# Kernel tuning notes

Measured on AMD Instinct MI355X. Metric: run time of the kernel, lower is better.

## Reference

```python
import jax, jax.numpy as jnp
import numpy as np

N_HEADS = 16

def setup_inputs() -> dict:
    key = jax.random.key(0)
    k1, k2, k3 = jax.random.split(key, 3)
    B, L, D = 2, 2048, 1024
    x = jax.random.normal(k1, (B, L, D), dtype=jnp.float32)
    w_qkv = jax.random.normal(k2, (D, 3 * D), dtype=jnp.float32) * (1.0 / np.sqrt(D))
    w_out = jax.random.normal(k3, (D, D), dtype=jnp.float32) * (1.0 / np.sqrt(D))
    return {"x": x, "w_qkv": w_qkv, "w_out": w_out}

def reference(x, w_qkv, w_out):
    B, L, D = x.shape
    H = N_HEADS
    dh = D // H
    qkv = x @ w_qkv                      # (B, L, 3D)
    q, k, v = jnp.split(qkv, 3, axis=-1)
    # (B, H, L, dh)
    q = q.reshape(B, L, H, dh).transpose(0, 2, 1, 3)
    k = k.reshape(B, L, H, dh).transpose(0, 2, 1, 3)
    v = v.reshape(B, L, H, dh).transpose(0, 2, 1, 3)
    scale = 1.0 / jnp.sqrt(jnp.asarray(dh, x.dtype))
    attn = jnp.einsum('bhqd,bhkd->bhqk', q, k) * scale   # (B, H, L, L)
    causal = jnp.tril(jnp.ones((L, L), dtype=bool))
    attn = jnp.where(causal[None, None], attn, -jnp.inf)
    attn = jax.nn.softmax(attn, axis=-1)
    out = jnp.einsum('bhqk,bhkd->bhqd', attn, v)         # (B, H, L, dh)
    out = out.transpose(0, 2, 1, 3).reshape(B, L, D)
    return out @ w_out
```

## Files before the change

### kernel.cpp

```cpp
#include <hip/hip_runtime.h>

typedef __attribute__((ext_vector_type(4))) float f32x4;
typedef __attribute__((ext_vector_type(16))) float f32x16;
typedef __attribute__((ext_vector_type(8))) __bf16 bf16x8;
typedef __attribute__((ext_vector_type(4))) __bf16 bf16x4;
typedef __attribute__((ext_vector_type(4))) unsigned u32x4;
typedef __attribute__((ext_vector_type(2))) unsigned u32x2;

static __device__ __forceinline__ f32x4 mfma16(bf16x8 a, bf16x8 b, f32x4 c) {
    return __builtin_amdgcn_mfma_f32_16x16x32_bf16(a, b, c, 0, 0, 0);
}
static __device__ __forceinline__ f32x16 mfma32(bf16x8 a, bf16x8 b, f32x16 c) {
    return __builtin_amdgcn_mfma_f32_32x32x16_bf16(a, b, c, 0, 0, 0);
}
static __device__ __forceinline__ unsigned pk_bf16(float a, float b) {
    unsigned lo = __builtin_bit_cast(unsigned short, (__bf16)a);
    unsigned hh = __builtin_bit_cast(unsigned short, (__bf16)b);
    return lo | (hh << 16);
}

#define QSCALE 0.18033688f
#define FENCE() asm volatile("" ::: "memory")
#define SYNCB()                          \
    do {                                 \
        FENCE();                         \
        __builtin_amdgcn_s_barrier();    \
        FENCE();                         \
    } while (0)

__global__ __launch_bounds__(256) void prep_all(const float* __restrict__ x,
                                                __bf16* __restrict__ xb,
                                                const float* __restrict__ wq,
                                                __bf16* __restrict__ wqT,
                                                const float* __restrict__ wo,
                                                __bf16* __restrict__ woT) {
    __shared__ float t[32][33];
    int bid = blockIdx.x, tid = threadIdx.x;
    if (bid < 4096) {
        int i = bid * 256 + tid;
        f32x4 v = ((const f32x4*)x)[i];
        bf16x4 o;
#pragma unroll
        for (int j = 0; j < 4; j++) o[j] = (__bf16)v[j];
        ((bf16x4*)xb)[i] = o;
        return;
    }
    const float* in;
    __bf16* out;
    int R, C, bx, by;
    if (bid < 4096 + 3072) {
        int b2 = bid - 4096;
        in = wq; out = wqT; R = 1024; C = 3072;
        bx = (b2 % 96) * 32; by = (b2 / 96) * 32;
    } else {
        int b2 = bid - 7168;
        in = wo; out = woT; R = 1024; C = 1024;
        bx = (b2 % 32) * 32; by = (b2 / 32) * 32;
    }
    int tx = tid & 31, ty = tid >> 5;
#pragma unroll
    for (int k = 0; k < 32; k += 8)
        t[ty + k][tx] = in[(size_t)(by + ty + k) * C + bx + tx];
    __syncthreads();
#pragma unroll
    for (int k = 0; k < 32; k += 8)
        out[(size_t)(bx + ty + k) * R + by + tx] = (__bf16)t[tx][ty + k];
}

__global__ __launch_bounds__(512, 2) void qkv_gemm8(const __bf16* __restrict__ A,
                                                    const __bf16* __restrict__ Bt,
                                                    __bf16* __restrict__ Qf,
                                                    __bf16* __restrict__ Kf,
                                                    __bf16* __restrict__ Vf) {
    const int K = 1024, NT = 16, MT = 12;
    __shared__ __attribute__((aligned(16))) __bf16 smem[65536];
    int tid = threadIdx.x;
    int w = tid >> 6, lane = tid & 63;
    int lrow = lane & 15, lgrp = lane >> 4;
    int wm = w >> 2, wn = w & 3;
    int bid = blockIdx.x;
    int swz = (bid & 7) * 24 + (bid >> 3);
    int m0 = (swz % MT) * 256, n0 = (swz / MT) * 256;

    int schunk = ((lane & 3) ^ ((lane >> 3) & 3)) * 8;
    const __bf16* aS[2];
    const __bf16* bS[2];
    int dstRow[2];
#pragma unroll
    for (int l = 0; l < 2; l++) {
        int r = w * 32 + l * 16 + (lane >> 2);
        aS[l] = A + (size_t)(m0 + r) * K + schunk;
        bS[l] = Bt + (size_t)(n0 + r) * K + schunk;
        dstRow[l] = (w * 32 + l * 16) * 64;
    }

    auto STAGE = [&](int h, int tt) {
        int tc = tt < NT ? tt : NT - 1;
        int op = h & 1, kh = h >> 1;
        int base = ((tt & 1) << 16) + (kh << 15) + (op << 14);
#pragma unroll
        for (int l = 0; l < 2; l++) {
            const __bf16* src = (op ? bS[l] : aS[l]) + tc * 64 + kh * 32;
            __builtin_amdgcn_global_load_lds(
                (const __attribute__((address_space(1))) void*)src,
                (__attribute__((address_space(3))) void*)(smem +
                                                          ((base + dstRow[l]) >> 1)),
                16, 0, 0);
        }
    };

    int swzsel = (lgrp ^ ((lrow >> 1) & 3)) << 4;
    auto RDA = [&](int buf, int kk, int row) {
        int off = (buf << 16) + (kk << 15) + row * 64 + swzsel;
        return *(const bf16x8*)(smem + (off >> 1));
    };
    auto RDB = [&](int buf, int kk, int row) {
        int off = (buf << 16) + (kk << 15) + 16384 + row * 64 + swzsel;
        return *(const bf16x8*)(smem + (off >> 1));
    };

    f32x4 acc[8][4];
#pragma unroll
    for (int i = 0; i < 8; i++)
#pragma unroll
        for (int j = 0; j < 4; j++) acc[i][j] = (f32x4){0.f, 0.f, 0.f, 0.f};
    bf16x8 bfr[4];

    STAGE(0, 0); STAGE(1, 0); STAGE(2, 0); STAGE(3, 0);
    STAGE(0, 1); STAGE(1, 1);
    asm volatile("s_waitcnt vmcnt(8)" ::: "memory");
    SYNCB();

#define PH(T, KKv, MHv, SH, ST, DOVM)                                          \
    {                                                                          \
        bf16x8 af[4];                                                          \
        if (MHv == 0) {                                                        \
            _Pragma("unroll") for (int nt = 0; nt < 4; nt++) bfr[nt] =         \
                RDB((T) & 1, KKv, wn * 64 + nt * 16 + lrow);                   \
        }                                                                      \
        _Pragma("unroll") for (int i = 0; i < 4; i++) af[i] =                  \
            RDA((T) & 1, KKv, wm * 128 + (MHv * 4 + i) * 16 + lrow);           \
        STAGE(SH, ST);                                                         \
        if (DOVM) asm volatile("s_waitcnt vmcnt(8)" ::: "memory");             \
        SYNCB();                                                               \
        asm volatile("s_waitcnt lgkmcnt(0)" ::: "memory");                     \
        __builtin_amdgcn_sched_barrier(0);                                     \
        __builtin_amdgcn_s_setprio(1);                                         \
        _Pragma("unroll") for (int i = 0; i < 4; i++)                          \
            _Pragma("unroll") for (int nt = 0; nt < 4; nt++)                   \
                acc[MHv * 4 + i][nt] =                                         \
                    mfma16(af[i], bfr[nt], acc[MHv * 4 + i][nt]);              \
        __builtin_amdgcn_s_setprio(0);                                         \
        SYNCB();                                                               \
    }

#pragma unroll 2
    for (int t = 0; t < NT; ++t) {
        PH(t, 0, 0, 2, t + 1, 0);
        PH(t, 0, 1, 3, t + 1, 1);
        PH(t, 1, 0, 0, t + 2, 0);
        PH(t, 1, 1, 1, t + 2, 1);
    }
#undef PH

    asm volatile("s_waitcnt vmcnt(0)" ::: "memory");
    SYNCB();

#pragma unroll
    for (int mt = 0; mt < 8; mt++) {
#pragma unroll
        for (int nt = 0; nt < 4; nt++) {
            int f0 = m0 + wm * 128 + mt * 16 + lgrp * 4;
            int t = n0 + wn * 64 + nt * 16 + lrow;
            int which = f0 >> 10, hn = f0 & 1023;
            int h = hn >> 6, d0 = hn & 63;
            int b = t >> 11, li = t & 2047;
            int bh = b * 16 + h, c = li >> 5, tl = li & 31;
            size_t bhbase = (size_t)bh * 131072;
            if (which == 2) {
                int ks = tl >> 4, hv = (tl >> 3) & 1, jv = tl & 7;
                size_t base =
                    bhbase + ((size_t)(c * 4 + ks * 2 + hv) * 64 + d0) * 8 + jv;
#pragma unroll
                for (int r = 0; r < 4; r++)
                    Vf[base + (size_t)r * 8] = (__bf16)acc[mt][nt][r];
            } else {
                int st = d0 >> 4, hv = (d0 >> 3) & 1, j0 = d0 & 7;
                size_t idx =
                    bhbase + ((size_t)(c * 8 + st * 2 + hv) * 32 + tl) * 8 + j0;
                bf16x4 pv;
                if (which == 0) {
#pragma unroll
                    for (int r = 0; r < 4; r++)
                        pv[r] = (__bf16)(acc[mt][nt][r] * QSCALE);
                    *(bf16x4*)(Qf + idx) = pv;
                } else {
#pragma unroll
                    for (int r = 0; r < 4; r++) pv[r] = (__bf16)acc[mt][nt][r];
                    *(bf16x4*)(Kf + idx) = pv;
                }
            }
        }
    }
}

#define BN 128
#define BKG 64

template <int MODE, int BMv>
__global__ __launch_bounds__(256) void gemm_bt(const __bf16* __restrict__ A,
                                               const __bf16* __restrict__ Bt,
                                               int M, int N, int K,
                                               float* __restrict__ Cout) {
    constexpr int nMt = BMv / 32;
    __shared__ __attribute__((aligned(16))) __bf16 As[BMv * BKG];
    __shared__ __attribute__((aligned(16))) __bf16 Bs[BN * BKG];
    int tid = threadIdx.x;
    int wave = tid >> 6, lane = tid & 63;
    int lrow = lane & 15, lgrp = lane >> 4;
    int bid = blockIdx.x;
    int chunk = gridDim.x >> 3;
    int swz = (bid & 7) * chunk + (bid >> 3);
    int nbx = N >> 7;
    int m0 = (swz / nbx) * BMv;
    int n0 = (swz % nbx) * BN;
    int wm = (wave >> 1) * (BMv / 2);
    int wn = (wave & 1) * 64;

    f32x4 acc[nMt][4];
#pragma unroll
    for (int i = 0; i < nMt; i++)
#pragma unroll
        for (int j = 0; j < 4; j++) acc[i][j] = (f32x4){0.f, 0.f, 0.f, 0.f};

    int srow = tid >> 3;
    int gch = (tid & 7) ^ (srow & 7);
    const __bf16* aSrc = A + (size_t)(m0 + srow) * K + gch * 8;
    const __bf16* bSrc = Bt + (size_t)(n0 + srow) * K + gch * 8;

    for (int k0 = 0; k0 < K; k0 += BKG) {
#pragma unroll
        for (int c = 0; c < BMv / 32; c++) {
            __builtin_amdgcn_global_load_lds(
                (const __attribute__((address_space(1))) void*)(aSrc + k0 + (size_t)c * 32 * K),
                (__attribute__((address_space(3))) void*)(As + (c * 256 + wave * 64) * 8),
                16, 0, 0);
        }
#pragma unroll
        for (int c = 0; c < 4; c++) {
            __builtin_amdgcn_global_load_lds(
                (const __attribute__((address_space(1))) void*)(bSrc + k0 + (size_t)c * 32 * K),
                (__attribute__((address_space(3))) void*)(Bs + (c * 256 + wave * 64) * 8),
                16, 0, 0);
        }
        __syncthreads();
#pragma unroll
        for (int kk = 0; kk < 2; kk++) {
            bf16x8 af[nMt], bfr[4];
#pragma unroll
            for (int mt = 0; mt < nMt; mt++) {
                int row = wm + mt * 16 + lrow;
                int slot = row * 8 + ((4 * kk + lgrp) ^ (row & 7));
                af[mt] = *(const bf16x8*)(As + slot * 8);
            }
#pragma unroll
            for (int nt = 0; nt < 4; nt++) {
                int row = wn + nt * 16 + lrow;
                int slot = row * 8 + ((4 * kk + lgrp) ^ (row & 7));
                bfr[nt] = *(const bf16x8*)(Bs + slot * 8);
            }
#pragma unroll
            for (int mt = 0; mt < nMt; mt++)
#pragma unroll
                for (int nt = 0; nt < 4; nt++)
                    acc[mt][nt] = mfma16(af[mt], bfr[nt], acc[mt][nt]);
        }
        __syncthreads();
    }

#pragma unroll
    for (int mt = 0; mt < nMt; mt++) {
#pragma unroll
        for (int nt = 0; nt < 4; nt++) {
            int f0 = m0 + wm + mt * 16 + lgrp * 4;
            int t = n0 + wn + nt * 16 + lrow;
            *(f32x4*)(Cout + (size_t)t * M + f0) = acc[mt][nt];
        }
    }
}

template <bool MASKED>
static __device__ __forceinline__ void attn_chunk(
    int c, int ql, int hi, const __bf16* __restrict__ Kp,
    const __bf16* __restrict__ Vp, const bf16x8 (&qf)[4], bf16x8 ones,
    f32x16& o0, f32x16& o1, f32x16& lsa) {
    const __bf16* kb = Kp + ((size_t)c * 8 + hi) * 256 + ql * 8;
    bf16x8 kf[4];
#pragma unroll
    for (int st = 0; st < 4; st++) kf[st] = *(const bf16x8*)(kb + st * 512);
    const __bf16* vb = Vp + ((size_t)c * 4 + hi) * 512 + ql * 8;
    bf16x8 v00 = *(const bf16x8*)(vb);
    bf16x8 v01 = *(const bf16x8*)(vb + 256);
    bf16x8 v10 = *(const bf16x8*)(vb + 1024);
    bf16x8 v11 = *(const bf16x8*)(vb + 1280);

    f32x16 sa;
#pragma unroll
    for (int r = 0; r < 16; r++) sa[r] = 0.f;
#pragma unroll
    for (int st = 0; st < 4; st++) sa = mfma32(kf[st], qf[st], sa);

    unsigned w[8];
#pragma unroll
    for (int i = 0; i < 8; i++) {
        float a = sa[2 * i], b = sa[2 * i + 1];
        if (MASKED) {
            int ra = 2 * i, rb = 2 * i + 1;
            if (((ra & 3) + 8 * (ra >> 2) + 4 * hi) > ql) a = -1e30f;
            if (((rb & 3) + 8 * (rb >> 2) + 4 * hi) > ql) b = -1e30f;
        }
        w[i] = pk_bf16(__builtin_amdgcn_exp2f(a), __builtin_amdgcn_exp2f(b));
    }
    u32x2 r02 = __builtin_amdgcn_permlane32_swap(w[0], w[2], false, false);
    u32x2 r13 = __builtin_amdgcn_permlane32_swap(w[1], w[3], false, false);
    u32x2 r46 = __builtin_amdgcn_permlane32_swap(w[4], w[6], false, false);
    u32x2 r57 = __builtin_amdgcn_permlane32_swap(w[5], w[7], false, false);
    bf16x8 pa0 = __builtin_bit_cast(bf16x8, (u32x4){r02[0], r13[0], r02[1], r13[1]});
    bf16x8 pa1 = __builtin_bit_cast(bf16x8, (u32x4){r46[0], r57[0], r46[1], r57[1]});

    o0 = mfma32(pa0, v00, o0);
    o1 = mfma32(pa0, v01, o1);
    lsa = mfma32(pa0, ones, lsa);
    o0 = mfma32(pa1, v10, o0);
    o1 = mfma32(pa1, v11, o1);
    lsa = mfma32(pa1, ones, lsa);
}

__global__ __launch_bounds__(256, 4) void attn_fwd15(const __bf16* __restrict__ Qf,
                                                     const __bf16* __restrict__ Kf,
                                                     const __bf16* __restrict__ Vf,
                                                     __bf16* __restrict__ Ob) {
    __shared__ float comb[2][64][49];
    int tid = threadIdx.x;
    int wave = tid >> 6, lane = tid & 63;
    int ql = lane & 31, hi = lane >> 5;
    int bid = blockIdx.x;
    int xcd = bid & 7, idx = bid >> 3;
    int bh = xcd * 4 + (idx >> 6);
    int strip = 63 - (idx & 63);
    int q0 = strip * 32;

    const __bf16* Qp = Qf + (size_t)bh * 131072;
    const __bf16* Kp = Kf + (size_t)bh * 131072;
    const __bf16* Vp = Vf + (size_t)bh * 131072;

    const __bf16* qb = Qp + ((size_t)strip * 8 + hi) * 256 + ql * 8;
    bf16x8 qf[4];
#pragma unroll
    for (int st = 0; st < 4; st++) qf[st] = *(const bf16x8*)(qb + st * 512);

    bf16x8 ones;
#pragma unroll
    for (int j = 0; j < 8; j++) ones[j] = (__bf16)1.0f;

    f32x16 o0, o1, lsa;
#pragma unroll
    for (int r = 0; r < 16; r++) { o0[r] = 0.f; o1[r] = 0.f; lsa[r] = 0.f; }

    for (int c = wave; c < strip; c += 4)
        attn_chunk<false>(c, ql, hi, Kp, Vp, qf, ones, o0, o1, lsa);
    if ((strip & 3) == wave)
        attn_chunk<true>(strip, ql, hi, Kp, Vp, qf, ones, o0, o1, lsa);

    if (wave >= 2) {
        float* sl = &comb[wave - 2][lane][0];
#pragma unroll
        for (int r = 0; r < 16; r++) {
            sl[r] = o0[r]; sl[16 + r] = o1[r]; sl[32 + r] = lsa[r];
        }
    }
    __syncthreads();
    if (wave < 2) {
        const float* sl = &comb[wave][lane][0];
#pragma unroll
        for (int r = 0; r < 16; r++) {
            o0[r] += sl[r]; o1[r] += sl[16 + r]; lsa[r] += sl[32 + r];
        }
    }
    __syncthreads();
    if (wave == 1) {
        float* sl = &comb[0][lane][0];
#pragma unroll
        for (int r = 0; r < 16; r++) {
            sl[r] = o0[r]; sl[16 + r] = o1[r]; sl[32 + r] = lsa[r];
        }
    }
    __syncthreads();
    if (wave == 0) {
        const float* sl = &comb[0][lane][0];
#pragma unroll
        for (int r = 0; r < 16; r++) {
            o0[r] += sl[r]; o1[r] += sl[16 + r]; lsa[r] += sl[32 + r];
        }
        int b = bh >> 4, h = bh & 15;
#pragma unroll
        for (int r = 0; r < 16; r++) {
            int crow = (r & 3) + 8 * (r >> 2) + 4 * hi;
            float inv;
            asm("v_rcp_f32 %0, %1" : "=v"(inv) : "v"(lsa[r]));
            size_t base = ((size_t)(b * 2048 + q0 + crow)) * 1024 + h * 64;
            Ob[base + ql] = (__bf16)(o0[r] * inv);
            Ob[base + 32 + ql] = (__bf16)(o1[r] * inv);
        }
    }
}

extern "C" void kernel_launch(void* const* d_in, const int* in_sizes, int n_in,
                              void* d_out, int out_size, void* d_ws, size_t ws_size,
                              hipStream_t stream) {
    const float* x = (const float*)d_in[0];
    const float* w_qkv = (const float*)d_in[1];
    const float* w_out = (const float*)d_in[2];
    float* out = (float*)d_out;

    char* ws = (char*)d_ws;
    __bf16* xb    = (__bf16*)(ws);
    __bf16* wqkvT = (__bf16*)(ws + (size_t)(8  << 20));
    __bf16* woutT = (__bf16*)(ws + (size_t)(14 << 20));
    __bf16* Qf    = (__bf16*)(ws + (size_t)(16 << 20));
    __bf16* Kf    = (__bf16*)(ws + (size_t)(24 << 20));
    __bf16* Vf    = (__bf16*)(ws + (size_t)(32 << 20));
    __bf16* Ob    = (__bf16*)(ws + (size_t)(40 << 20));

    prep_all<<<8192, 256, 0, stream>>>(x, xb, w_qkv, wqkvT, w_out, woutT);
    qkv_gemm8<<<192, 512, 0, stream>>>(wqkvT, xb, Qf, Kf, Vf);
    attn_fwd15<<<2048, 256, 0, stream>>>(Qf, Kf, Vf, Ob);
    gemm_bt<0, 64><<<512, 256, 0, stream>>>(
        woutT, Ob, 1024, 4096, 1024, out);
}
```

Baseline: 94.79 us.

## Process two query strips per attention block to reuse K/V fragments

Each attention block now handles two adjacent 32-row query strips, so every K/V chunk loaded from global memory feeds both strips' QK and PV matrix multiplies. The grid is halved, launch bounds drop to 2 blocks per CU, and the shared-memory reduction buffer doubles to combine both strips' accumulators. This targets K/V load traffic and per-block overhead, in exchange for higher register pressure, lower occupancy and coarser load balancing across the causal triangle.

```diff
diff --git a/kernel.cpp b/kernel.cpp
--- a/kernel.cpp
+++ b/kernel.cpp
@@ -290,20 +290,10 @@
 }
 
 template <bool MASKED>
-static __device__ __forceinline__ void attn_chunk(
-    int c, int ql, int hi, const __bf16* __restrict__ Kp,
-    const __bf16* __restrict__ Vp, const bf16x8 (&qf)[4], bf16x8 ones,
+static __device__ __forceinline__ void strip_qkpv(
+    int ql, int hi, const bf16x8 (&kf)[4], bf16x8 v00, bf16x8 v01,
+    bf16x8 v10, bf16x8 v11, const bf16x8 (&qf)[4], bf16x8 ones,
     f32x16& o0, f32x16& o1, f32x16& lsa) {
-    const __bf16* kb = Kp + ((size_t)c * 8 + hi) * 256 + ql * 8;
-    bf16x8 kf[4];
-#pragma unroll
-    for (int st = 0; st < 4; st++) kf[st] = *(const bf16x8*)(kb + st * 512);
-    const __bf16* vb = Vp + ((size_t)c * 4 + hi) * 512 + ql * 8;
-    bf16x8 v00 = *(const bf16x8*)(vb);
-    bf16x8 v01 = *(const bf16x8*)(vb + 256);
-    bf16x8 v10 = *(const bf16x8*)(vb + 1024);
-    bf16x8 v11 = *(const bf16x8*)(vb + 1280);
-
     f32x16 sa;
 #pragma unroll
     for (int r = 0; r < 16; r++) sa[r] = 0.f;
@@ -336,81 +326,125 @@
     lsa = mfma32(pa1, ones, lsa);
 }
 
-__global__ __launch_bounds__(256, 4) void attn_fwd15(const __bf16* __restrict__ Qf,
+__global__ __launch_bounds__(256, 2) void attn_fwd16(const __bf16* __restrict__ Qf,
                                                      const __bf16* __restrict__ Kf,
                                                      const __bf16* __restrict__ Vf,
                                                      __bf16* __restrict__ Ob) {
-    __shared__ float comb[2][64][49];
+    __shared__ float comb[2][2][64][49];
     int tid = threadIdx.x;
     int wave = tid >> 6, lane = tid & 63;
     int ql = lane & 31, hi = lane >> 5;
     int bid = blockIdx.x;
     int xcd = bid & 7, idx = bid >> 3;
-    int bh = xcd * 4 + (idx >> 6);
-    int strip = 63 - (idx & 63);
-    int q0 = strip * 32;
+    int bh = xcd * 4 + (idx >> 5);
+    int T = 31 - (idx & 31);
+    int S0 = 2 * T, S1 = S0 + 1;
 
     const __bf16* Qp = Qf + (size_t)bh * 131072;
     const __bf16* Kp = Kf + (size_t)bh * 131072;
     const __bf16* Vp = Vf + (size_t)bh * 131072;
 
-    const __bf16* qb = Qp + ((size_t)strip * 8 + hi) * 256 + ql * 8;
-    bf16x8 qf[4];
-#pragma unroll
-    for (int st = 0; st < 4; st++) qf[st] = *(const bf16x8*)(qb + st * 512);
+    bf16x8 qf0[4], qf1[4];
+    {
+        const __bf16* qb0 = Qp + ((size_t)S0 * 8 + hi) * 256 + ql * 8;
+        const __bf16* qb1 = Qp + ((size_t)S1 * 8 + hi) * 256 + ql * 8;
+#pragma unroll
+        for (int st = 0; st < 4; st++) {
+            qf0[st] = *(const bf16x8*)(qb0 + st * 512);
+            qf1[st] = *(const bf16x8*)(qb1 + st * 512);
+        }
+    }
 
     bf16x8 ones;
 #pragma unroll
     for (int j = 0; j < 8; j++) ones[j] = (__bf16)1.0f;
 
-    f32x16 o0, o1, lsa;
-#pragma unroll
-    for (int r = 0; r < 16; r++) { o0[r] = 0.f; o1[r] = 0.f; lsa[r] = 0.f; }
-
-    for (int c = wave; c < strip; c += 4)
-        attn_chunk<false>(c, ql, hi, Kp, Vp, qf, ones, o0, o1, lsa);
-    if ((strip & 3) == wave)
-        attn_chunk<true>(strip, ql, hi, Kp, Vp, qf, ones, o0, o1, lsa);
+    f32x16 oa0, oa1, la, ob0, ob1, lb;
+#pragma unroll
+    for (int r = 0; r < 16; r++) {
+        oa0[r] = 0.f; oa1[r] = 0.f; la[r] = 0.f;
+        ob0[r] = 0.f; ob1[r] = 0.f; lb[r] = 0.f;
+    }
+
+#define LOADKV(c)                                                       \
+    const __bf16* kb = Kp + ((size_t)(c)*8 + hi) * 256 + ql * 8;        \
+    bf16x8 kf[4];                                                       \
+    _Pragma("unroll") for (int st = 0; st < 4; st++) kf[st] =           \
+        *(const bf16x8*)(kb + st * 512);                                \
+    const __bf16* vb = Vp + ((size_t)(c)*4 + hi) * 512 + ql * 8;        \
+    bf16x8 v00 = *(const bf16x8*)(vb);                                  \
+    bf16x8 v01 = *(const bf16x8*)(vb + 256);                            \
+    bf16x8 v10 = *(const bf16x8*)(vb + 1024);                           \
+    bf16x8 v11 = *(const bf16x8*)(vb + 1280);
+
+    for (int c = wave; c < S0; c += 4) {
+        LOADKV(c);
+        strip_qkpv<false>(ql, hi, kf, v00, v01, v10, v11, qf0, ones, oa0, oa1, la);
+        strip_qkpv<false>(ql, hi, kf, v00, v01, v10, v11, qf1, ones, ob0, ob1, lb);
+    }
+    if ((S0 & 3) == wave) {
+        LOADKV(S0);
+        strip_qkpv<true>(ql, hi, kf, v00, v01, v10, v11, qf0, ones, oa0, oa1, la);
+        strip_qkpv<false>(ql, hi, kf, v00, v01, v10, v11, qf1, ones, ob0, ob1, lb);
+    }
+    if ((S1 & 3) == wave) {
+        LOADKV(S1);
+        strip_qkpv<true>(ql, hi, kf, v00, v01, v10, v11, qf1, ones, ob0, ob1, lb);
+    }
+#undef LOADKV
 
     if (wave >= 2) {
-        float* sl = &comb[wave - 2][lane][0];
+        float* s0 = &comb[wave - 2][0][lane][0];
+        float* s1 = &comb[wave - 2][1][lane][0];
 #pragma unroll
         for (int r = 0; r < 16; r++) {
-            sl[r] = o0[r]; sl[16 + r] = o1[r]; sl[32 + r] = lsa[r];
+            s0[r] = oa0[r]; s0[16 + r] = oa1[r]; s0[32 + r] = la[r];
+            s1[r] = ob0[r]; s1[16 + r] = ob1[r]; s1[32 + r] = lb[r];
         }
     }
     __syncthreads();
     if (wave < 2) {
-        const float* sl = &comb[wave][lane][0];
+        const float* s0 = &comb[wave][0][lane][0];
+        const float* s1 = &comb[wave][1][lane][0];
 #pragma unroll
         for (int r = 0; r < 16; r++) {
-            o0[r] += sl[r]; o1[r] += sl[16 + r]; lsa[r] += sl[32 + r];
+            oa0[r] += s0[r]; oa1[r] += s0[16 + r]; la[r] += s0[32 + r];
+            ob0[r] += s1[r]; ob1[r] += s1[16 + r]; lb[r] += s1[32 + r];
         }
     }
     __syncthreads();
     if (wave == 1) {
-        float* sl = &comb[0][lane][0];
+        float* s0 = &comb[0][0][lane][0];
+        float* s1 = &comb[0][1][lane][0];
 #pragma unroll
         for (int r = 0; r < 16; r++) {
-            sl[r] = o0[r]; sl[16 + r] = o1[r]; sl[32 + r] = lsa[r];
+            s0[r] = oa0[r]; s0[16 + r] = oa1[r]; s0[32 + r] = la[r];
+            s1[r] = ob0[r]; s1[16 + r] = ob1[r]; s1[32 + r] = lb[r];
         }
     }
     __syncthreads();
     if (wave == 0) {
-        const float* sl = &comb[0][lane][0];
+        const float* s0 = &comb[0][0][lane][0];
+        const float* s1 = &comb[0][1][lane][0];
 #pragma unroll
         for (int r = 0; r < 16; r++) {
-            o0[r] += sl[r]; o1[r] += sl[16 + r]; lsa[r] += sl[32 + r];
+            oa0[r] += s0[r]; oa1[r] += s0[16 + r]; la[r] += s0[32 + r];
+            ob0[r] += s1[r]; ob1[r] += s1[16 + r]; lb[r] += s1[32 + r];
         }
         int b = bh >> 4, h = bh & 15;
+        int q00 = S0 * 32, q01 = S1 * 32;
 #pragma unroll
         for (int r = 0; r < 16; r++) {
             int crow = (r & 3) + 8 * (r >> 2) + 4 * hi;
-            float inv;
-            asm("v_rcp_f32 %0, %1" : "=v"(inv) : "v"(lsa[r]));
-            size_t base = ((size_t)(b * 2048 + q0 + crow)) * 1024 + h * 64;
-            Ob[base + ql] = (__bf16)(o0[r] * inv);
-            Ob[base + 32 + ql] = (__bf16)(o1[r] * inv);
+            float inv0, inv1;
+            asm("v_rcp_f32 %0, %1" : "=v"(inv0) : "v"(la[r]));
+            asm("v_rcp_f32 %0, %1" : "=v"(inv1) : "v"(lb[r]));
+            size_t b0 = ((size_t)(b * 2048 + q00 + crow)) * 1024 + h * 64;
+            size_t b1 = ((size_t)(b * 2048 + q01 + crow)) * 1024 + h * 64;
+            Ob[b0 + ql] = (__bf16)(oa0[r] * inv0);
+            Ob[b0 + 32 + ql] = (__bf16)(oa1[r] * inv0);
+            Ob[b1 + ql] = (__bf16)(ob0[r] * inv1);
+            Ob[b1 + 32 + ql] = (__bf16)(ob1[r] * inv1);
         }
     }
 }
@@ -434,7 +468,7 @@
 
     prep_all<<<8192, 256, 0, stream>>>(x, xb, w_qkv, wqkvT, w_out, woutT);
     qkv_gemm8<<<192, 512, 0, stream>>>(wqkvT, xb, Qf, Kf, Vf);
-    attn_fwd15<<<2048, 256, 0, stream>>>(Qf, Kf, Vf, Ob);
+    attn_fwd16<<<1024, 256, 0, stream>>>(Qf, Kf, Vf, Ob);
     gemm_bt<0, 64><<<512, 256, 0, stream>>>(
         woutT, Ob, 1024, 4096, 1024, out);
 }
```

Result: slower. 97.76 us (+3.1%).
